# Kernel optimization log

Measured on AMD Instinct MI355X. Metric: run time of the kernel, lower is better.

The kernel has to match this reference:

```python
import jax, jax.numpy as jnp
import numpy as np

N_ENT = 100000
N_REL = 500
IN_DIM = 128
OUT_DIM = 128
N_TRIP = 250000
BN_EPS = 1e-5
LRELU_SLOPE = 0.01


def setup_inputs() -> dict:
    key = jax.random.key(0)
    ks = jax.random.split(key, 10)
    heads = jax.random.randint(ks[0], (N_TRIP, 1), 0, N_ENT, dtype=jnp.int32)
    tails = jax.random.randint(ks[1], (N_TRIP, 1), 0, N_ENT, dtype=jnp.int32)
    rels = jax.random.randint(ks[2], (N_TRIP, 1), 0, N_REL, dtype=jnp.int32)
    triplets = jnp.concatenate([heads, tails, rels], axis=1)
    embed_range = (6.0 + 2.0) / OUT_DIM  # (margin + epsilon) / out_dim
    ent_embed = jax.random.uniform(ks[3], (N_ENT, IN_DIM), jnp.float32, -embed_range, embed_range)
    rel_embed = jax.random.uniform(ks[4], (N_REL, IN_DIM), jnp.float32, -embed_range, embed_range)
    a_w = jax.random.normal(ks[5], (OUT_DIM, 3 * IN_DIM), jnp.float32) * (1.414 * (2.0 / (3 * IN_DIM + OUT_DIM)) ** 0.5)
    a_b = jnp.zeros((OUT_DIM,), jnp.float32)
    a2_w = jax.random.normal(ks[6], (1, OUT_DIM), jnp.float32) * (1.414 * (2.0 / (OUT_DIM + 1)) ** 0.5)
    a2_b = jnp.zeros((1,), jnp.float32)
    return dict(
        triplets=triplets,
        ent_embed=ent_embed,
        rel_embed=rel_embed,
        a_w=a_w,
        a_b=a_b,
        a2_w=a2_w,
        a2_b=a2_b,
        bn0_g=jnp.ones((3 * IN_DIM,), jnp.float32),
        bn0_b=jnp.zeros((3 * IN_DIM,), jnp.float32),
        bn1_g=jnp.ones((OUT_DIM,), jnp.float32),
        bn1_b=jnp.zeros((OUT_DIM,), jnp.float32),
    )


def _batchnorm(x, gamma, beta):
    # training-mode BN: batch statistics over axis 0, biased variance
    mean = jnp.mean(x, axis=0)
    var = jnp.mean(jnp.square(x - mean), axis=0)
    return (x - mean) * jax.lax.rsqrt(var + BN_EPS) * gamma + beta


def _leaky_relu(x):
    return jnp.where(x >= 0, x, LRELU_SLOPE * x)


def reference(triplets, ent_embed, rel_embed, a_w, a_b, a2_w, a2_b,
              bn0_g, bn0_b, bn1_g, bn1_b):
    t0, t1, t2 = triplets[:, 0], triplets[:, 1], triplets[:, 2]
    e0 = ent_embed[t0]           # [n, in_dim]
    e1 = ent_embed[t1]           # [n, in_dim]
    r = rel_embed[t2]            # [n, in_dim]
    h_fwd = jnp.concatenate([e0, e1, r], axis=1)    # [n, 3*in_dim]
    h_bwd = jnp.concatenate([e1, e0, -r], axis=1)   # [n, 3*in_dim]
    h = jnp.concatenate([h_fwd, h_bwd], axis=0)     # [2n, 3*in_dim]
    h = _batchnorm(h, bn0_g, bn0_b)                 # dropout omitted (eval)
    c = _batchnorm(h @ a_w.T + a_b, bn1_g, bn1_b)   # [2n, out_dim]
    b = -_leaky_relu(c @ a2_w.T + a2_b)             # [2n, 1]
    e_b = jnp.exp(b)                                # [2n, 1]

    # edges[0] = cat(t0, t1); scatter-add messages into source node slots
    seg = jnp.concatenate([t0, t1], axis=0)         # [2n]
    temp1 = e_b * c                                 # [2n, out_dim]
    ebs = jax.ops.segment_sum(e_b, seg, num_segments=N_ENT)    # [N, 1]
    hs = jax.ops.segment_sum(temp1, seg, num_segments=N_ENT)   # [N, out_dim]
    ebs = jnp.where(ebs == 0, 1e-12, ebs)
    h_ent = hs / ebs                                # [N, out_dim]

    # scatter-mean of forward-direction messages by relation id
    rel_sum = jax.ops.segment_sum(temp1[:N_TRIP], t2, num_segments=N_REL)
    rel_cnt = jax.ops.segment_sum(jnp.ones((N_TRIP, 1), temp1.dtype), t2, num_segments=N_REL)
    h_rel = rel_sum / jnp.maximum(rel_cnt, 1.0)     # [R, out_dim]
    return h_ent, h_rel
```

## Files before the change

kernel.cpp:

```cpp
#include <hip/hip_runtime.h>
#include <hip/hip_bf16.h>

#define NE 100000
#define NR 500
#define DD 128
#define NT 250000
#define NEV 500000
#define RELOFF 12800000
#define TWO_NF 500000.0f
#define NTF 250000.0f
#define TBH 2048
#define NBH ((NT + TBH - 1)/TBH)
#define NBS ((NE + 1023)/1024)

typedef __attribute__((ext_vector_type(8))) short short8;
typedef __attribute__((ext_vector_type(4))) float f32x4;

__device__ __forceinline__ float bf2f(unsigned short u){
  unsigned int x = ((unsigned int)u) << 16;
  return __uint_as_float(x);
}
__device__ __forceinline__ float bf2f_lo(unsigned int u){ return __uint_as_float(u << 16); }
__device__ __forceinline__ float bf2f_hi(unsigned int u){ return __uint_as_float(u & 0xFFFF0000u); }
__device__ __forceinline__ unsigned short f2bf(float f){
  __hip_bfloat16 h = __float2bfloat16(f);
  return *reinterpret_cast<unsigned short*>(&h);
}
__device__ __forceinline__ void atomAddF(float* p, float v){ unsafeAtomicAdd(p, v); }
__device__ __forceinline__ float wredsum(float x){
  x += __shfl_xor(x, 1, 64);  x += __shfl_xor(x, 2, 64);  x += __shfl_xor(x, 4, 64);
  x += __shfl_xor(x, 8, 64);  x += __shfl_xor(x, 16, 64); x += __shfl_xor(x, 32, 64);
  return x;
}

__global__ __launch_bounds__(256) void k_hist(const int* __restrict__ trip,
                                              int* __restrict__ cnt, int* __restrict__ gHist){
  __shared__ int h[NR];
  int t = threadIdx.x;
  for (int r = t; r < NR; r += 256) h[r] = 0;
  __syncthreads();
  int b0 = blockIdx.x*TBH, b1 = min(b0+TBH, NT);
  for (int i = b0 + t; i < b1; i += 256){
    int t0 = trip[3*i], t1 = trip[3*i+1], t2 = trip[3*i+2];
    atomicAdd(&cnt[t0], 1);
    atomicAdd(&cnt[t1], 1);
    atomicAdd(&h[t2], 1);
  }
  __syncthreads();
  for (int r = t; r < NR; r += 256) gHist[blockIdx.x*NR + r] = h[r];
}

__global__ __launch_bounds__(512) void k_histscan(const int* __restrict__ gHist,
                                                  int* __restrict__ base, int* __restrict__ cntR,
                                                  int* __restrict__ offR){
  __shared__ int sm[512];
  int r = threadIdx.x;
  int s = 0;
  if (r < NR){
    for (int b = 0; b < NBH; ++b){ base[b*NR + r] = s; s += gHist[b*NR + r]; }
    cntR[r] = s;
  }
  sm[r] = (r < NR) ? s : 0;
  __syncthreads();
  for (int st = 1; st < 512; st <<= 1){
    int x = (r >= st) ? sm[r-st] : 0;
    __syncthreads();
    sm[r] += x;
    __syncthreads();
  }
  if (r < NR){
    int off = sm[r] - s;
    offR[r] = off;
    for (int b = 0; b < NBH; ++b) base[b*NR + r] += off;
  }
  if (r == 0) offR[NR] = NT;
}

__global__ __launch_bounds__(1024) void k_scan1(const int* __restrict__ cnt,
                                                int* __restrict__ off, int* __restrict__ bsum){
  __shared__ int wsum[16];
  int t = threadIdx.x, lane = t & 63, w = t >> 6;
  int i = blockIdx.x*1024 + t;
  int v = (i < NE) ? cnt[i] : 0;
  int x = v;
  #pragma unroll
  for (int s = 1; s < 64; s <<= 1){ int y = __shfl_up(x, s, 64); if (lane >= s) x += y; }
  if (lane == 63) wsum[w] = x;
  __syncthreads();
  if (w == 0 && lane < 16){
    int xs = wsum[lane];
    #pragma unroll
    for (int s = 1; s < 16; s <<= 1){ int y = __shfl_up(xs, s, 16); if ((lane & 15) >= s) xs += y; }
    wsum[lane] = xs;
  }
  __syncthreads();
  int wprev = (w == 0) ? 0 : wsum[w-1];
  int incl = wprev + x;
  if (i < NE) off[i] = incl - v;
  if (t == 1023) bsum[blockIdx.x] = incl;
}

__global__ __launch_bounds__(128) void k_scan2(const int* __restrict__ bsum,
                                               int* __restrict__ bbase, int* __restrict__ off){
  __shared__ int sm[128];
  int t = threadIdx.x;
  int v = (t < NBS) ? bsum[t] : 0;
  sm[t] = v; __syncthreads();
  for (int s = 1; s < 128; s <<= 1){
    int x = (t >= s) ? sm[t-s] : 0;
    __syncthreads();
    sm[t] += x;
    __syncthreads();
  }
  int incl = sm[t];
  if (t < NBS) bbase[t] = incl - v;
  if (t == NBS-1) off[NE] = incl;
}

__global__ __launch_bounds__(1024) void k_scan3(int* __restrict__ off, int* __restrict__ cur,
                                                const int* __restrict__ bbase){
  int i = blockIdx.x*1024 + threadIdx.x;
  if (i < NE){
    int o = off[i] + bbase[blockIdx.x];
    off[i] = o;
    cur[i] = o;
  }
}

__global__ void k_scat_ent(const int* __restrict__ trip, int* __restrict__ curE,
                           unsigned long long* __restrict__ evE){
  int i = blockIdx.x*blockDim.x + threadIdx.x;
  if (i < NT){
    int t0 = trip[3*i+0], t1 = trip[3*i+1], t2 = trip[3*i+2];
    int p0 = atomicAdd(&curE[t0], 1);
    unsigned long long e0 = (unsigned)t0 |
      ((unsigned long long)(((unsigned)t1 << 10) | ((unsigned)t2 << 1)) << 32);
    __builtin_nontemporal_store(e0, &evE[p0]);
    int p1 = atomicAdd(&curE[t1], 1);
    unsigned long long e1 = (unsigned)t1 |
      ((unsigned long long)(((unsigned)t0 << 10) | ((unsigned)t2 << 1) | 1u) << 32);
    __builtin_nontemporal_store(e1, &evE[p1]);
  }
}

__global__ __launch_bounds__(256) void k_scat_rel(const int* __restrict__ trip,
                                                  const int* __restrict__ base,
                                                  unsigned long long* __restrict__ evR){
  __shared__ int cur[NR];
  int t = threadIdx.x;
  for (int r = t; r < NR; r += 256) cur[r] = base[blockIdx.x*NR + r];
  __syncthreads();
  int b0 = blockIdx.x*TBH, b1 = min(b0+TBH, NT);
  for (int i = b0 + t; i < b1; i += 256){
    int t0 = trip[3*i], t1 = trip[3*i+1], t2 = trip[3*i+2];
    int p = atomicAdd(&cur[t2], 1);
    unsigned long long e = (unsigned)t0 | ((unsigned long long)(unsigned)t1 << 32);
    __builtin_nontemporal_store(e, &evR[p]);
  }
}

__global__ __launch_bounds__(256) void k_entstats(const float* __restrict__ ent, const int* __restrict__ cnt,
                                                  float* __restrict__ S, float* __restrict__ Q){
  int j = threadIdx.x & 127;
  int half = threadIdx.x >> 7;
  int r0 = blockIdx.x*128 + half;
  int r1 = min(blockIdx.x*128 + 128, NE);
  float s = 0.f, q = 0.f;
  for (int r = r0; r < r1; r += 2){
    int w = cnt[r];
    if (w){
      float x = ent[(size_t)r*DD + j];
      float wf = (float)w;
      s += wf*x; q += wf*x*x;
    }
  }
  __shared__ float ss[256], qq[256];
  ss[threadIdx.x] = s; qq[threadIdx.x] = q; __syncthreads();
  if (half == 0){
    atomAddF(&S[j], ss[j] + ss[j+128]);
    atomAddF(&Q[j], qq[j] + qq[j+128]);
  }
}

__global__ void k_alpha(const float* __restrict__ rel, const int* __restrict__ cntR,
                        const float* __restrict__ S, const float* __restrict__ Q,
                        const float* __restrict__ bn0g, const float* __restrict__ bn0b,
                        float* __restrict__ alpha0, float* __restrict__ alpha1, float* __restrict__ alpha2,
                        float* __restrict__ beta0, float* __restrict__ beta1){
  int j = threadIdx.x;
  float qr = 0.f;
  for (int k = 0; k < NR; ++k){
    float w = (float)cntR[k];
    float x = rel[k*DD + j];
    qr += w*x*x;
  }
  float mean = S[j] / TWO_NF;
  float var  = Q[j] / TWO_NF - mean*mean;
  float inv  = rsqrtf(var + 1e-5f);
  float a0 = inv * bn0g[j];
  float a1 = inv * bn0g[128+j];
  alpha0[j] = a0; alpha1[j] = a1;
  beta0[j] = bn0b[j]     - mean*a0;
  beta1[j] = bn0b[128+j] - mean*a1;
  float varR = qr / NTF;
  alpha2[j] = rsqrtf(varR + 1e-5f) * bn0g[256+j];
}

__global__ void k_bias(const float* __restrict__ aw, const float* __restrict__ ab,
                       const float* __restrict__ bn0b,
                       const float* __restrict__ beta0, const float* __restrict__ beta1,
                       float* __restrict__ bias){
  int o = blockIdx.x, j = threadIdx.x;
  const float* r = aw + (size_t)o*384;
  float p = r[j]*beta0[j] + r[128+j]*beta1[j] + r[256+j]*bn0b[256+j];
  __shared__ float sm[128];
  sm[j] = p; __syncthreads();
  for (int s = 64; s > 0; s >>= 1){ if (j < s) sm[j] += sm[j+s]; __syncthreads(); }
  if (j == 0) bias[o] = ab[o] + sm[0];
}

__global__ void k_v(const float* __restrict__ rel, const float* __restrict__ aw,
                    const float* __restrict__ alpha2, float* __restrict__ V){
  int k = blockIdx.x, o = threadIdx.x;
  __shared__ float rl[128];
  rl[o] = rel[k*DD + o] * alpha2[o];
  __syncthreads();
  float acc = 0.f;
  #pragma unroll 8
  for (int j = 0; j < 128; ++j) acc += aw[(size_t)o*384 + 256 + j] * rl[j];
  V[k*DD + o] = acc;
}

__global__ void k_wfold2(const float* __restrict__ aw, const float* __restrict__ alpha0,
                         const float* __restrict__ alpha1, unsigned short* __restrict__ Wt2){
  int o = blockIdx.x;
  int k = threadIdx.x;
  float w;
  if (o < 128) w = aw[(size_t)o*384 + k] * alpha0[k];
  else         w = aw[(size_t)(o-128)*384 + 128 + k] * alpha1[k];
  Wt2[(size_t)o*128 + k] = f2bf(w);
}

__global__ __launch_bounds__(256) void k_u2(const float* __restrict__ ent,
                                            const unsigned short* __restrict__ Wt2,
                                            unsigned short* __restrict__ Uo){
  __shared__ unsigned short stg[4][16*264];
  int tid = threadIdx.x;
  int w = tid >> 6, l = tid & 63;
  int col = l & 15, grp = l >> 4, kof = grp*8;
  int e0w = (blockIdx.x*4 + w)*16;
  int e = min(e0w + col, NE-1);
  const float* xrow = ent + (size_t)e*DD;

  short8 a_hi0, a_hi1, a_hi2, a_hi3, a_lo0, a_lo1, a_lo2, a_lo3;
  {
    #pragma unroll
    for (int ks = 0; ks < 4; ++ks){
      float4 xa = *(const float4*)(xrow + 32*ks + kof);
      float4 xb = *(const float4*)(xrow + 32*ks + kof + 4);
      float xv[8] = {xa.x, xa.y, xa.z, xa.w, xb.x, xb.y, xb.z, xb.w};
      short8 hi, lo;
      #pragma unroll
      for (int j = 0; j < 8; ++j){
        unsigned short h = f2bf(xv[j]);
        unsigned short r = f2bf(xv[j] - bf2f(h));
        hi[j] = (short)h; lo[j] = (short)r;
      }
      if (ks == 0){ a_hi0 = hi; a_lo0 = lo; }
      else if (ks == 1){ a_hi1 = hi; a_lo1 = lo; }
      else if (ks == 2){ a_hi2 = hi; a_lo2 = lo; }
      else { a_hi3 = hi; a_lo3 = lo; }
    }
  }

  f32x4 acc[16];
  #pragma unroll
  for (int ot = 0; ot < 16; ++ot) acc[ot] = (f32x4){0.f, 0.f, 0.f, 0.f};

  #pragma unroll
  for (int ot = 0; ot < 16; ++ot){
    const unsigned short* bbase = Wt2 + (size_t)(ot*16 + col)*128 + kof;
    short8 b0 = *(const short8*)(bbase);
    short8 b1 = *(const short8*)(bbase + 32);
    short8 b2 = *(const short8*)(bbase + 64);
    short8 b3 = *(const short8*)(bbase + 96);
    acc[ot] = __builtin_amdgcn_mfma_f32_16x16x32_bf16(a_hi0, b0, acc[ot], 0, 0, 0);
    acc[ot] = __builtin_amdgcn_mfma_f32_16x16x32_bf16(a_lo0, b0, acc[ot], 0, 0, 0);
    acc[ot] = __builtin_amdgcn_mfma_f32_16x16x32_bf16(a_hi1, b1, acc[ot], 0, 0, 0);
    acc[ot] = __builtin_amdgcn_mfma_f32_16x16x32_bf16(a_lo1, b1, acc[ot], 0, 0, 0);
    acc[ot] = __builtin_amdgcn_mfma_f32_16x16x32_bf16(a_hi2, b2, acc[ot], 0, 0, 0);
    acc[ot] = __builtin_amdgcn_mfma_f32_16x16x32_bf16(a_lo2, b2, acc[ot], 0, 0, 0);
    acc[ot] = __builtin_amdgcn_mfma_f32_16x16x32_bf16(a_hi3, b3, acc[ot], 0, 0, 0);
    acc[ot] = __builtin_amdgcn_mfma_f32_16x16x32_bf16(a_lo3, b3, acc[ot], 0, 0, 0);
  }

  #pragma unroll
  for (int ot = 0; ot < 16; ++ot){
    #pragma unroll
    for (int r = 0; r < 4; ++r){
      stg[w][(grp*4 + r)*264 + ot*16 + col] = f2bf(acc[ot][r]);
    }
  }
  #pragma unroll
  for (int i = 0; i < 16; ++i){
    if (e0w + i < NE){
      ushort4 v = ((const ushort4*)&stg[w][i*264])[l];
      ((ushort4*)Uo)[(size_t)(e0w + i)*64 + l] = v;
    }
  }
}

__global__ __launch_bounds__(256) void k_c1b(const uint2* __restrict__ evE,
                   const unsigned short* __restrict__ U, const float* __restrict__ V,
                   const float* __restrict__ bias,
                   float* __restrict__ colsum, float* __restrict__ colsumsq){
  int lane = threadIdx.x & 63;
  int w = threadIdx.x >> 6;
  int wv = blockIdx.x*4 + w;
  int nwv = gridDim.x*4;
  int per = (NEV + nwv - 1) / nwv;
  int st = wv*per, en = min(st + per, NEV);
  int c0 = 2*lane, c1 = c0+1;
  float b0 = bias[c0], b1 = bias[c1];
  const ushort2* Ub = (const ushort2*)U;
  const float2*  Vp = (const float2*)V;
  float s0=0.f, s1=0.f, q0=0.f, q1=0.f;
  for (int bs = st; bs < en; bs += 64){
    int n = min(64, en - bs);
    uint2 ev = (bs + lane < en) ? evE[bs + lane] : make_uint2(0u, 0u);
    int j = 0;
    for (; j + 2 <= n; j += 2){
      unsigned ow0 = __shfl(ev.x, j, 64),   pk0 = __shfl(ev.y, j, 64);
      unsigned ow1 = __shfl(ev.x, j+1, 64), pk1 = __shfl(ev.y, j+1, 64);
      ushort2 a0 = Ub[(size_t)ow0*128 + lane];
      ushort2 g0 = Ub[(size_t)(pk0 >> 10)*128 + 64 + lane];
      float2  v0 = Vp[((pk0 >> 1) & 0x1FF)*64 + lane];
      ushort2 a1 = Ub[(size_t)ow1*128 + lane];
      ushort2 g1 = Ub[(size_t)(pk1 >> 10)*128 + 64 + lane];
      float2  v1 = Vp[((pk1 >> 1) & 0x1FF)*64 + lane];
      float sg0 = (pk0 & 1) ? -1.f : 1.f;
      float sg1 = (pk1 & 1) ? -1.f : 1.f;
      float y00 = bf2f(a0.x) + bf2f(g0.x) + sg0*v0.x + b0;
      float y01 = bf2f(a0.y) + bf2f(g0.y) + sg0*v0.y + b1;
      float y10 = bf2f(a1.x) + bf2f(g1.x) + sg1*v1.x + b0;
      float y11 = bf2f(a1.y) + bf2f(g1.y) + sg1*v1.y + b1;
      s0 += y00 + y10;  q0 += y00*y00 + y10*y10;
      s1 += y01 + y11;  q1 += y01*y01 + y11*y11;
    }
    for (; j < n; ++j){
      unsigned ow0 = __shfl(ev.x, j, 64), pk0 = __shfl(ev.y, j, 64);
      ushort2 a0 = Ub[(size_t)ow0*128 + lane];
      ushort2 g0 = Ub[(size_t)(pk0 >> 10)*128 + 64 + lane];
      float2  v0 = Vp[((pk0 >> 1) & 0x1FF)*64 + lane];
      float sg0 = (pk0 & 1) ? -1.f : 1.f;
      float y00 = bf2f(a0.x) + bf2f(g0.x) + sg0*v0.x + b0;
      float y01 = bf2f(a0.y) + bf2f(g0.y) + sg0*v0.y + b1;
      s0 += y00;  q0 += y00*y00;
      s1 += y01;  q1 += y01*y01;
    }
  }
  __shared__ float sred[4][128], qred[4][128];
  sred[w][c0] = s0; sred[w][c1] = s1;
  qred[w][c0] = q0; qred[w][c1] = q1;
  __syncthreads();
  int t = threadIdx.x;
  if (t < 128){
    atomAddF(&colsum[t],   sred[0][t] + sred[1][t] + sred[2][t] + sred[3][t]);
    atomAddF(&colsumsq[t], qred[0][t] + qred[1][t] + qred[2][t] + qred[3][t]);
  }
}

__global__ void k_bn1fin(const float* __restrict__ colsum, const float* __restrict__ colsumsq,
                         const float* __restrict__ bn1g, const float* __restrict__ bn1b,
                         const float* __restrict__ a2w, const float* __restrict__ a2b,
                         const float* __restrict__ biasv,
                         float* __restrict__ A1, float* __restrict__ B1,
                         float* __restrict__ a2A, float* __restrict__ sbase){
  int j = threadIdx.x;
  float mean = colsum[j] / TWO_NF;
  float var  = colsumsq[j] / TWO_NF - mean*mean;
  float A = rsqrtf(var + 1e-5f) * bn1g[j];
  float B = bn1b[j] - mean*A;
  A1[j] = A; B1[j] = B;
  float w2 = a2w[j];
  float aA = w2*A;
  a2A[j] = aA;
  __shared__ float sm[128], sm2[128];
  sm[j] = w2*B; sm2[j] = biasv[j]*aA;
  __syncthreads();
  for (int s = 64; s > 0; s >>= 1){
    if (j < s){ sm[j] += sm[j+s]; sm2[j] += sm2[j+s]; }
    __syncthreads();
  }
  if (j == 0){
    float sb = a2b[0] + sm[0];
    sbase[0] = sb;
    sbase[1] = sb + sm2[0];
  }
}

__global__ __launch_bounds__(256) void k_sigma(const unsigned short* __restrict__ U,
                                               const float* __restrict__ a2A,
                                               float* __restrict__ sig){
  int lane = threadIdx.x & 63;
  int e = blockIdx.x*4 + (threadIdx.x>>6);
  if (e >= NE) return;
  const uint2* Ur = (const uint2*)U;
  uint2 r = Ur[(size_t)e*64 + lane];
  int c = (lane & 31)*4;
  float4 w = *(const float4*)&a2A[c];
  float p = bf2f_lo(r.x)*w.x + bf2f_hi(r.x)*w.y + bf2f_lo(r.y)*w.z + bf2f_hi(r.y)*w.w;
  p += __shfl_xor(p, 1, 64); p += __shfl_xor(p, 2, 64); p += __shfl_xor(p, 4, 64);
  p += __shfl_xor(p, 8, 64); p += __shfl_xor(p, 16, 64);
  if ((lane & 31) == 0) sig[2*e + (lane >> 5)] = p;
}

__global__ __launch_bounds__(256) void k_rho(const float* __restrict__ V,
                                             const float* __restrict__ a2A,
                                             float* __restrict__ rho){
  int lane = threadIdx.x & 63;
  int k = blockIdx.x*4 + (threadIdx.x>>6);
  if (k >= NR) return;
  const float2* Vp = (const float2*)V;
  float2 v = Vp[(size_t)k*64 + lane];
  int c0 = 2*lane;
  float p = v.x*a2A[c0] + v.y*a2A[c0+1];
  p = wredsum(p);
  if (lane == 0) rho[k] = p;
}

__global__ __launch_bounds__(256) void k_gent(const uint2* __restrict__ evE, const int* __restrict__ offE,
                   const unsigned short* __restrict__ U, const float* __restrict__ V,
                   const float* __restrict__ sig, const float* __restrict__ rho,
                   const float* __restrict__ bias,
                   const float* __restrict__ A1, const float* __restrict__ B1,
                   const float* __restrict__ sbase,
                   float* __restrict__ out){
  int lane = threadIdx.x & 63;
  int e = blockIdx.x*4 + (threadIdx.x>>6);
  if (e >= NE) return;
  int c0 = 2*lane, c1 = c0+1;
  const ushort2* Ub = (const ushort2*)U;
  const float2*  Vp = (const float2*)V;
  ushort2 u0 = Ub[(size_t)e*128 + lane];
  float base0 = bf2f(u0.x) + bias[c0], base1 = bf2f(u0.y) + bias[c1];
  float pb  = sbase[1];
  float s0e = sig[2*e];
  float accU0=0.f, accU1=0.f, accV0=0.f, accV1=0.f, sep=0.f;
  int p0 = offE[e], p1 = offE[e+1];
  for (int bs = p0; bs < p1; bs += 64){
    int n = min(64, p1 - bs);
    unsigned ev = 0u; float ebl = 0.f;
    if (bs + lane < p1){
      ev = evE[bs + lane].y;
      int oth = ev >> 10, rl = (ev >> 1) & 0x1FF;
      float sg = (ev & 1) ? -1.f : 1.f;
      float s = s0e + sig[2*oth + 1] + sg*rho[rl] + pb;
      float bb = (s >= 0.f) ? -s : -0.01f*s;
      ebl = expf(bb);
    }
    sep += ebl;
    int j = 0;
    for (; j + 2 <= n; j += 2){
      unsigned e0 = __shfl(ev, j, 64);
      unsigned e1 = __shfl(ev, j+1, 64);
      float eb0 = __shfl(ebl, j, 64);
      float eb1 = __shfl(ebl, j+1, 64);
      ushort2 g0 = Ub[(size_t)(e0 >> 10)*128 + 64 + lane];
      ushort2 g1 = Ub[(size_t)(e1 >> 10)*128 + 64 + lane];
      float2 v0 = Vp[((e0 >> 1) & 0x1FF)*64 + lane];
      float2 v1 = Vp[((e1 >> 1) & 0x1FF)*64 + lane];
      float w0 = (e0 & 1) ? -eb0 : eb0;
      float w1 = (e1 & 1) ? -eb1 : eb1;
      accU0 += eb0*bf2f(g0.x); accU1 += eb0*bf2f(g0.y);
      accV0 += w0*v0.x;        accV1 += w0*v0.y;
      accU0 += eb1*bf2f(g1.x); accU1 += eb1*bf2f(g1.y);
      accV0 += w1*v1.x;        accV1 += w1*v1.y;
    }
    for (; j < n; ++j){
      unsigned e0 = __shfl(ev, j, 64);
      float eb0 = __shfl(ebl, j, 64);
      ushort2 g0 = Ub[(size_t)(e0 >> 10)*128 + 64 + lane];
      float2 v0 = Vp[((e0 >> 1) & 0x1FF)*64 + lane];
      float w0 = (e0 & 1) ? -eb0 : eb0;
      accU0 += eb0*bf2f(g0.x); accU1 += eb0*bf2f(g0.y);
      accV0 += w0*v0.x;        accV1 += w0*v0.y;
    }
  }
  float se = wredsum(sep);
  float sY0 = se*base0 + accU0 + accV0;
  float sY1 = se*base1 + accU1 + accV1;
  float hs0 = A1[c0]*sY0 + B1[c0]*se;
  float hs1 = A1[c1]*sY1 + B1[c1]*se;
  float d = (se == 0.f) ? 1e-12f : se;
  out[(size_t)e*DD + c0] = hs0/d;
  out[(size_t)e*DD + c1] = hs1/d;
}

__global__ __launch_bounds__(256) void k_grel(const uint2* __restrict__ evR, const int* __restrict__ offR,
                   const unsigned short* __restrict__ U, const float* __restrict__ V,
                   const float* __restrict__ sig, const float* __restrict__ rho,
                   const float* __restrict__ bias,
                   const float* __restrict__ A1, const float* __restrict__ B1,
                   const float* __restrict__ sbase,
                   float* __restrict__ out){
  int lane = threadIdx.x & 63;
  int k = blockIdx.x >> 3;
  int wvs = (blockIdx.x & 7)*4 + (threadIdx.x >> 6);
  int c0 = 2*lane, c1 = c0+1;
  const ushort2* Ub = (const ushort2*)U;
  const float2*  Vp = (const float2*)V;
  float2 v = Vp[(size_t)k*64 + lane];
  float vb0 = v.x + bias[c0], vb1 = v.y + bias[c1];
  float rpb = rho[k] + sbase[1];
  float accY0=0.f, accY1=0.f, sep=0.f;
  int p0 = offR[k], p1 = offR[k+1];
  int tot = p1 - p0, per = (tot + 31) >> 5;
  int st = p0 + wvs*per, en = min(st + per, p1);
  for (int bs = st; bs < en; bs += 64){
    int n = min(64, en - bs);
    uint2 ev = make_uint2(0u, 0u); float ebl = 0.f;
    if (bs + lane < en){
      ev = evR[bs + lane];
      float s = sig[2*ev.x] + sig[2*ev.y + 1] + rpb;
      float bb = (s >= 0.f) ? -s : -0.01f*s;
      ebl = expf(bb);
    }
    sep += ebl;
    int j = 0;
    for (; j + 2 <= n; j += 2){
      unsigned a0 = __shfl(ev.x, j, 64),   d0 = __shfl(ev.y, j, 64);
      unsigned a1 = __shfl(ev.x, j+1, 64), d1 = __shfl(ev.y, j+1, 64);
      float eb0 = __shfl(ebl, j, 64);
      float eb1 = __shfl(ebl, j+1, 64);
      ushort2 ua0 = Ub[(size_t)a0*128 + lane];
      ushort2 ud0 = Ub[(size_t)d0*128 + 64 + lane];
      ushort2 ua1 = Ub[(size_t)a1*128 + lane];
      ushort2 ud1 = Ub[(size_t)d1*128 + 64 + lane];
      accY0 += eb0*(bf2f(ua0.x) + bf2f(ud0.x));
      accY1 += eb0*(bf2f(ua0.y) + bf2f(ud0.y));
      accY0 += eb1*(bf2f(ua1.x) + bf2f(ud1.x));
      accY1 += eb1*(bf2f(ua1.y) + bf2f(ud1.y));
    }
    for (; j < n; ++j){
      unsigned a0 = __shfl(ev.x, j, 64), d0 = __shfl(ev.y, j, 64);
      float eb0 = __shfl(ebl, j, 64);
      ushort2 ua0 = Ub[(size_t)a0*128 + lane];
      ushort2 ud0 = Ub[(size_t)d0*128 + 64 + lane];
      accY0 += eb0*(bf2f(ua0.x) + bf2f(ud0.x));
      accY1 += eb0*(bf2f(ua0.y) + bf2f(ud0.y));
    }
  }
  float se = wredsum(sep);
  float sY0 = accY0 + se*vb0;
  float sY1 = accY1 + se*vb1;
  float r0 = A1[c0]*sY0 + B1[c0]*se;
  float r1 = A1[c1]*sY1 + B1[c1]*se;
  atomAddF(&out[(size_t)RELOFF + (size_t)k*DD + c0], r0);
  atomAddF(&out[(size_t)RELOFF + (size_t)k*DD + c1], r1);
}

__global__ void k_fin_rel(float* __restrict__ out, const int* __restrict__ cntR){
  int idx = blockIdx.x*blockDim.x + threadIdx.x;
  int k = idx >> 7;
  float c = fmaxf((float)cntR[k], 1.f);
  out[RELOFF + idx] = out[RELOFF + idx] / c;
}

extern "C" void kernel_launch(void* const* d_in, const int* in_sizes, int n_in,
                              void* d_out, int out_size, void* d_ws, size_t ws_size,
                              hipStream_t stream) {
  (void)in_sizes; (void)n_in; (void)ws_size; (void)out_size;
  const int*   trip = (const int*)  d_in[0];
  const float* ent  = (const float*)d_in[1];
  const float* rel  = (const float*)d_in[2];
  const float* aw   = (const float*)d_in[3];
  const float* ab   = (const float*)d_in[4];
  const float* a2w  = (const float*)d_in[5];
  const float* a2b  = (const float*)d_in[6];
  const float* bn0g = (const float*)d_in[7];
  const float* bn0b = (const float*)d_in[8];
  const float* bn1g = (const float*)d_in[9];
  const float* bn1b = (const float*)d_in[10];
  float* out = (float*)d_out;

  char* w = (char*)d_ws;
  size_t off = 0;
  auto take = [&](size_t bytes) -> char* {
    char* p = w + off;
    off = (off + bytes + 511) & ~(size_t)511;
    return p;
  };
  float* S        = (float*)take(512);
  float* Q        = (float*)take(512);
  float* colsum   = (float*)take(512);
  float* colsumsq = (float*)take(512);
  int*   cnt      = (int*)  take((size_t)NE*4);
  size_t zero_end = off;
  int*   cntR   = (int*)  take((size_t)NR*4);
  float* alpha0 = (float*)take(512);
  float* alpha1 = (float*)take(512);
  float* alpha2 = (float*)take(512);
  float* beta0  = (float*)take(512);
  float* beta1  = (float*)take(512);
  float* biasv  = (float*)take(512);
  float* A1     = (float*)take(512);
  float* B1     = (float*)take(512);
  float* a2A    = (float*)take(512);
  float* sbase  = (float*)take(512);
  float* rho    = (float*)take((size_t)NR*4);
  float* sig    = (float*)take((size_t)NE*2*4);
  int*   offE   = (int*)  take((size_t)(NE+1)*4);
  int*   curE   = (int*)  take((size_t)NE*4);
  int*   offR   = (int*)  take((size_t)(NR+1)*4);
  int*   gHist  = (int*)  take((size_t)NBH*NR*4);
  int*   gBase  = (int*)  take((size_t)NBH*NR*4);
  int*   bsum   = (int*)  take((size_t)NBS*4);
  int*   bbase  = (int*)  take((size_t)NBS*4);
  unsigned long long* evE = (unsigned long long*)take((size_t)NEV*8);
  unsigned long long* evR = (unsigned long long*)take((size_t)NT*8);
  float* V      = (float*)take((size_t)NR*DD*4);
  unsigned short* Wt2 = (unsigned short*)take((size_t)256*128*2);
  unsigned short* U   = (unsigned short*)take((size_t)NE*256*2);

  hipMemsetAsync((char*)d_out + (size_t)RELOFF*4, 0, (size_t)NR*DD*4, stream);
  hipMemsetAsync(d_ws, 0, zero_end, stream);

  k_hist     <<<NBH, 256, 0, stream>>>(trip, cnt, gHist);
  k_histscan <<<1, 512, 0, stream>>>(gHist, gBase, cntR, offR);
  k_scan1    <<<NBS, 1024, 0, stream>>>(cnt, offE, bsum);
  k_scan2    <<<1, 128, 0, stream>>>(bsum, bbase, offE);
  k_scan3    <<<NBS, 1024, 0, stream>>>(offE, curE, bbase);
  k_scat_ent <<<(NT+255)/256, 256, 0, stream>>>(trip, curE, evE);
  k_scat_rel <<<NBH, 256, 0, stream>>>(trip, gBase, evR);
  k_entstats <<<(NE+127)/128, 256, 0, stream>>>(ent, cnt, S, Q);
  k_alpha    <<<1, 128, 0, stream>>>(rel, cntR, S, Q, bn0g, bn0b, alpha0, alpha1, alpha2, beta0, beta1);
  k_bias     <<<128, 128, 0, stream>>>(aw, ab, bn0b, beta0, beta1, biasv);
  k_v        <<<NR, 128, 0, stream>>>(rel, aw, alpha2, V);
  k_wfold2   <<<256, 128, 0, stream>>>(aw, alpha0, alpha1, Wt2);
  k_u2       <<<1563, 256, 0, stream>>>(ent, Wt2, U);
  k_c1b      <<<2048, 256, 0, stream>>>((const uint2*)evE, U, V, biasv, colsum, colsumsq);
  k_bn1fin   <<<1, 128, 0, stream>>>(colsum, colsumsq, bn1g, bn1b, a2w, a2b, biasv, A1, B1, a2A, sbase);
  k_sigma    <<<NE/4, 256, 0, stream>>>(U, a2A, sig);
  k_rho      <<<(NR+3)/4, 256, 0, stream>>>(V, a2A, rho);
  k_gent     <<<NE/4, 256, 0, stream>>>((const uint2*)evE, offE, U, V, sig, rho, biasv, A1, B1, sbase, out);
  k_grel     <<<NR*8, 256, 0, stream>>>((const uint2*)evR, offR, U, V, sig, rho, biasv, A1, B1, sbase, out);
  k_fin_rel  <<<(NR*DD)/256, 256, 0, stream>>>(out, cntR);
}
```

Measured before the change: 426.7 us.

## Drop bf16 hi/lo split in U GEMM and unroll gather loops by four

The entity projection GEMM no longer splits fp32 inputs into bf16 high and low parts. It does a single bf16 MFMA pass, which halves the MFMA count and the conversion work but loses input precision. Separately, the gather loops in the BN-statistics and aggregation kernels are unrolled from two edges to four per iteration. This puts more independent gathers in flight to hide memory latency, at the cost of extra registers.

```diff
diff --git a/kernel.cpp b/kernel.cpp
--- a/kernel.cpp
+++ b/kernel.cpp
@@ -252,24 +252,21 @@
   int e = min(e0w + col, NE-1);
   const float* xrow = ent + (size_t)e*DD;
 
-  short8 a_hi0, a_hi1, a_hi2, a_hi3, a_lo0, a_lo1, a_lo2, a_lo3;
+  short8 a0v, a1v, a2v, a3v;
   {
     #pragma unroll
     for (int ks = 0; ks < 4; ++ks){
       float4 xa = *(const float4*)(xrow + 32*ks + kof);
       float4 xb = *(const float4*)(xrow + 32*ks + kof + 4);
-      float xv[8] = {xa.x, xa.y, xa.z, xa.w, xb.x, xb.y, xb.z, xb.w};
-      short8 hi, lo;
-      #pragma unroll
-      for (int j = 0; j < 8; ++j){
-        unsigned short h = f2bf(xv[j]);
-        unsigned short r = f2bf(xv[j] - bf2f(h));
-        hi[j] = (short)h; lo[j] = (short)r;
-      }
-      if (ks == 0){ a_hi0 = hi; a_lo0 = lo; }
-      else if (ks == 1){ a_hi1 = hi; a_lo1 = lo; }
-      else if (ks == 2){ a_hi2 = hi; a_lo2 = lo; }
-      else { a_hi3 = hi; a_lo3 = lo; }
+      short8 hi;
+      hi[0] = (short)f2bf(xa.x); hi[1] = (short)f2bf(xa.y);
+      hi[2] = (short)f2bf(xa.z); hi[3] = (short)f2bf(xa.w);
+      hi[4] = (short)f2bf(xb.x); hi[5] = (short)f2bf(xb.y);
+      hi[6] = (short)f2bf(xb.z); hi[7] = (short)f2bf(xb.w);
+      if (ks == 0) a0v = hi;
+      else if (ks == 1) a1v = hi;
+      else if (ks == 2) a2v = hi;
+      else a3v = hi;
     }
   }
 
@@ -284,14 +281,10 @@
     short8 b1 = *(const short8*)(bbase + 32);
     short8 b2 = *(const short8*)(bbase + 64);
     short8 b3 = *(const short8*)(bbase + 96);
-    acc[ot] = __builtin_amdgcn_mfma_f32_16x16x32_bf16(a_hi0, b0, acc[ot], 0, 0, 0);
-    acc[ot] = __builtin_amdgcn_mfma_f32_16x16x32_bf16(a_lo0, b0, acc[ot], 0, 0, 0);
-    acc[ot] = __builtin_amdgcn_mfma_f32_16x16x32_bf16(a_hi1, b1, acc[ot], 0, 0, 0);
-    acc[ot] = __builtin_amdgcn_mfma_f32_16x16x32_bf16(a_lo1, b1, acc[ot], 0, 0, 0);
-    acc[ot] = __builtin_amdgcn_mfma_f32_16x16x32_bf16(a_hi2, b2, acc[ot], 0, 0, 0);
-    acc[ot] = __builtin_amdgcn_mfma_f32_16x16x32_bf16(a_lo2, b2, acc[ot], 0, 0, 0);
-    acc[ot] = __builtin_amdgcn_mfma_f32_16x16x32_bf16(a_hi3, b3, acc[ot], 0, 0, 0);
-    acc[ot] = __builtin_amdgcn_mfma_f32_16x16x32_bf16(a_lo3, b3, acc[ot], 0, 0, 0);
+    acc[ot] = __builtin_amdgcn_mfma_f32_16x16x32_bf16(a0v, b0, acc[ot], 0, 0, 0);
+    acc[ot] = __builtin_amdgcn_mfma_f32_16x16x32_bf16(a1v, b1, acc[ot], 0, 0, 0);
+    acc[ot] = __builtin_amdgcn_mfma_f32_16x16x32_bf16(a2v, b2, acc[ot], 0, 0, 0);
+    acc[ot] = __builtin_amdgcn_mfma_f32_16x16x32_bf16(a3v, b3, acc[ot], 0, 0, 0);
   }
 
   #pragma unroll
@@ -329,23 +322,39 @@
     int n = min(64, en - bs);
     uint2 ev = (bs + lane < en) ? evE[bs + lane] : make_uint2(0u, 0u);
     int j = 0;
-    for (; j + 2 <= n; j += 2){
+    for (; j + 4 <= n; j += 4){
       unsigned ow0 = __shfl(ev.x, j, 64),   pk0 = __shfl(ev.y, j, 64);
       unsigned ow1 = __shfl(ev.x, j+1, 64), pk1 = __shfl(ev.y, j+1, 64);
+      unsigned ow2 = __shfl(ev.x, j+2, 64), pk2 = __shfl(ev.y, j+2, 64);
+      unsigned ow3 = __shfl(ev.x, j+3, 64), pk3 = __shfl(ev.y, j+3, 64);
       ushort2 a0 = Ub[(size_t)ow0*128 + lane];
       ushort2 g0 = Ub[(size_t)(pk0 >> 10)*128 + 64 + lane];
       float2  v0 = Vp[((pk0 >> 1) & 0x1FF)*64 + lane];
       ushort2 a1 = Ub[(size_t)ow1*128 + lane];
       ushort2 g1 = Ub[(size_t)(pk1 >> 10)*128 + 64 + lane];
       float2  v1 = Vp[((pk1 >> 1) & 0x1FF)*64 + lane];
+      ushort2 a2 = Ub[(size_t)ow2*128 + lane];
+      ushort2 g2 = Ub[(size_t)(pk2 >> 10)*128 + 64 + lane];
+      float2  v2 = Vp[((pk2 >> 1) & 0x1FF)*64 + lane];
+      ushort2 a3 = Ub[(size_t)ow3*128 + lane];
+      ushort2 g3 = Ub[(size_t)(pk3 >> 10)*128 + 64 + lane];
+      float2  v3 = Vp[((pk3 >> 1) & 0x1FF)*64 + lane];
       float sg0 = (pk0 & 1) ? -1.f : 1.f;
       float sg1 = (pk1 & 1) ? -1.f : 1.f;
+      float sg2 = (pk2 & 1) ? -1.f : 1.f;
+      float sg3 = (pk3 & 1) ? -1.f : 1.f;
       float y00 = bf2f(a0.x) + bf2f(g0.x) + sg0*v0.x + b0;
       float y01 = bf2f(a0.y) + bf2f(g0.y) + sg0*v0.y + b1;
       float y10 = bf2f(a1.x) + bf2f(g1.x) + sg1*v1.x + b0;
       float y11 = bf2f(a1.y) + bf2f(g1.y) + sg1*v1.y + b1;
-      s0 += y00 + y10;  q0 += y00*y00 + y10*y10;
-      s1 += y01 + y11;  q1 += y01*y01 + y11*y11;
+      float y20 = bf2f(a2.x) + bf2f(g2.x) + sg2*v2.x + b0;
+      float y21 = bf2f(a2.y) + bf2f(g2.y) + sg2*v2.y + b1;
+      float y30 = bf2f(a3.x) + bf2f(g3.x) + sg3*v3.x + b0;
+      float y31 = bf2f(a3.y) + bf2f(g3.y) + sg3*v3.y + b1;
+      s0 += y00 + y10 + y20 + y30;
+      s1 += y01 + y11 + y21 + y31;
+      q0 += y00*y00 + y10*y10 + y20*y20 + y30*y30;
+      q1 += y01*y01 + y11*y11 + y21*y21 + y31*y31;
     }
     for (; j < n; ++j){
       unsigned ow0 = __shfl(ev.x, j, 64), pk0 = __shfl(ev.y, j, 64);
@@ -461,21 +470,35 @@
     }
     sep += ebl;
     int j = 0;
-    for (; j + 2 <= n; j += 2){
+    for (; j + 4 <= n; j += 4){
       unsigned e0 = __shfl(ev, j, 64);
       unsigned e1 = __shfl(ev, j+1, 64);
+      unsigned e2 = __shfl(ev, j+2, 64);
+      unsigned e3 = __shfl(ev, j+3, 64);
       float eb0 = __shfl(ebl, j, 64);
       float eb1 = __shfl(ebl, j+1, 64);
+      float eb2 = __shfl(ebl, j+2, 64);
+      float eb3 = __shfl(ebl, j+3, 64);
       ushort2 g0 = Ub[(size_t)(e0 >> 10)*128 + 64 + lane];
       ushort2 g1 = Ub[(size_t)(e1 >> 10)*128 + 64 + lane];
+      ushort2 g2 = Ub[(size_t)(e2 >> 10)*128 + 64 + lane];
+      ushort2 g3 = Ub[(size_t)(e3 >> 10)*128 + 64 + lane];
       float2 v0 = Vp[((e0 >> 1) & 0x1FF)*64 + lane];
       float2 v1 = Vp[((e1 >> 1) & 0x1FF)*64 + lane];
+      float2 v2 = Vp[((e2 >> 1) & 0x1FF)*64 + lane];
+      float2 v3 = Vp[((e3 >> 1) & 0x1FF)*64 + lane];
       float w0 = (e0 & 1) ? -eb0 : eb0;
       float w1 = (e1 & 1) ? -eb1 : eb1;
+      float w2 = (e2 & 1) ? -eb2 : eb2;
+      float w3 = (e3 & 1) ? -eb3 : eb3;
       accU0 += eb0*bf2f(g0.x); accU1 += eb0*bf2f(g0.y);
       accV0 += w0*v0.x;        accV1 += w0*v0.y;
       accU0 += eb1*bf2f(g1.x); accU1 += eb1*bf2f(g1.y);
       accV0 += w1*v1.x;        accV1 += w1*v1.y;
+      accU0 += eb2*bf2f(g2.x); accU1 += eb2*bf2f(g2.y);
+      accV0 += w2*v2.x;        accV1 += w2*v2.y;
+      accU0 += eb3*bf2f(g3.x); accU1 += eb3*bf2f(g3.y);
+      accV0 += w3*v3.x;        accV1 += w3*v3.y;
     }
     for (; j < n; ++j){
       unsigned e0 = __shfl(ev, j, 64);
```

After: 419.8 us. About the same (-1.6%).
